# Kernel tuning notes

Measured on AMD Instinct MI355X. Metric: run time of the kernel, lower is better.

The kernel has to match this reference:

```python
import jax, jax.numpy as jnp
import numpy as np

WS = (7, 7, 7)
N = WS[0] * WS[1] * WS[2]          # 343 tokens per window
B, D, L, H = 128, 512, 6, 8
DH = D // H                        # 64
DFF = 4 * D
EPS = 1e-5


def _relative_position_index_3d(ws):
    d = np.arange(ws[0]); h = np.arange(ws[1]); w = np.arange(ws[2])
    coords = np.stack(np.meshgrid(d, h, w, indexing='ij'))      # [3, D, H, W]
    cf = coords.reshape(3, -1)                                   # [3, n]
    rel = cf[:, :, None] - cf[:, None, :]                        # [3, n, n]
    rel = rel.transpose(1, 2, 0).copy()                          # [n, n, 3]
    rel[:, :, 0] += ws[0] - 1
    rel[:, :, 1] += ws[1] - 1
    rel[:, :, 2] += ws[2] - 1
    rel[:, :, 0] *= (2 * ws[1] - 1) * (2 * ws[2] - 1)
    rel[:, :, 1] *= 2 * ws[2] - 1
    return rel.sum(-1).astype(np.int32)                          # [n, n]


def setup_inputs() -> dict:
    key = jax.random.key(0)
    ks = jax.random.split(key, 16)
    s = lambda d: 1.0 / np.sqrt(d)
    inp = {
        'x':    jax.random.normal(ks[0], (B, N, D), jnp.float32),
        'Wq':   jax.random.normal(ks[1], (L, D, D), jnp.float32) * s(D),
        'Wk':   jax.random.normal(ks[2], (L, D, D), jnp.float32) * s(D),
        'Wv':   jax.random.normal(ks[3], (L, D, D), jnp.float32) * s(D),
        'Wo':   jax.random.normal(ks[4], (L, D, D), jnp.float32) * s(D),
        'W1ff': jax.random.normal(ks[5], (L, D, DFF), jnp.float32) * s(D),
        'b1ff': jnp.zeros((L, DFF), jnp.float32),
        'W2ff': jax.random.normal(ks[6], (L, DFF, D), jnp.float32) * s(DFF),
        'b2ff': jnp.zeros((L, D), jnp.float32),
        'ln1_g': jnp.ones((L, D), jnp.float32),
        'ln1_b': jnp.zeros((L, D), jnp.float32),
        'ln2_g': jnp.ones((L, D), jnp.float32),
        'ln2_b': jnp.zeros((L, D), jnp.float32),
        'lnf_g': jnp.ones((D,), jnp.float32),
        'lnf_b': jnp.zeros((D,), jnp.float32),
        'rel_table': jax.random.normal(ks[7], ((2 * WS[0] - 1) * (2 * WS[1] - 1) * (2 * WS[2] - 1), H), jnp.float32) * 0.02,
        'cpb_w1': jax.random.normal(ks[8], (H, 512), jnp.float32) * s(H),
        'cpb_b1': jax.random.normal(ks[9], (512,), jnp.float32) * 0.02,
        'cpb_w2': jax.random.normal(ks[10], (512, H), jnp.float32) * s(512),
        'rel_index': jnp.asarray(_relative_position_index_3d(WS)),
    }
    return inp


def _layer_norm(x, g, b):
    mu = jnp.mean(x, -1, keepdims=True)
    xc = x - mu
    var = jnp.mean(xc * xc, -1, keepdims=True)
    return xc * jax.lax.rsqrt(var + EPS) * g + b


def _rel_pos_bias(rel_table, cpb_w1, cpb_b1, cpb_w2, rel_index):
    # cpb_mlp: Linear(H->512) + ReLU + Linear(512->H, no bias)
    t = jax.nn.relu(rel_table @ cpb_w1 + cpb_b1) @ cpb_w2        # [T, H]
    bias = t[rel_index.reshape(-1)].reshape(N, N, H)             # gather -> [n, n, H]
    return jnp.transpose(bias, (2, 0, 1))                        # [H, n, n]


def reference(x, Wq, Wk, Wv, Wo, W1ff, b1ff, W2ff, b2ff,
              ln1_g, ln1_b, ln2_g, ln2_b, lnf_g, lnf_b,
              rel_table, cpb_w1, cpb_b1, cpb_w2, rel_index):
    bias = _rel_pos_bias(rel_table, cpb_w1, cpb_b1, cpb_w2, rel_index)  # [H, n, n] shared across layers
    scale = DH ** -0.5
    for l in range(L):
        # --- attention block (pre-norm) ---
        h = _layer_norm(x, ln1_g[l], ln1_b[l])
        q = (h @ Wq[l]).reshape(B, N, H, DH)
        k = (h @ Wk[l]).reshape(B, N, H, DH)
        v = (h @ Wv[l]).reshape(B, N, H, DH)
        scores = jnp.einsum('bihd,bjhd->bhij', q, k) * scale + bias[None]
        attn = jax.nn.softmax(scores, axis=-1)
        o = jnp.einsum('bhij,bjhd->bihd', attn, v).reshape(B, N, D)
        x = x + o @ Wo[l]
        # --- feed-forward block (pre-norm) ---
        h = _layer_norm(x, ln2_g[l], ln2_b[l])
        x = x + jax.nn.gelu(h @ W1ff[l] + b1ff[l]) @ W2ff[l] + b2ff[l]
    return _layer_norm(x, lnf_g, lnf_b)
```

## Files before the change

### kernel.cpp

```cpp
#include <hip/hip_runtime.h>

typedef __attribute__((ext_vector_type(8))) short short8;
typedef __attribute__((ext_vector_type(4))) float fx4;
typedef __attribute__((ext_vector_type(4))) int ix4;

#define MFMA16(a, b, c) __builtin_amdgcn_mfma_f32_16x16x32_bf16((a), (b), (c), 0, 0, 0)

__device__ __forceinline__ short f2bf(float f) {
  unsigned u = __float_as_uint(f);
  u += 0x7fffu + ((u >> 16) & 1u);
  return (short)(u >> 16);
}
__device__ __forceinline__ float bf2f(short v) {
  return __uint_as_float(((unsigned)(unsigned short)v) << 16);
}
__device__ __forceinline__ void glds16(const short* g, short* l) {
  __builtin_amdgcn_global_load_lds((const __attribute__((address_space(1))) void*)g,
                                   (__attribute__((address_space(3))) void*)l, 16, 0, 0);
}
__device__ __forceinline__ unsigned lds_off(const void* p) {
  return (unsigned)(uintptr_t)(const __attribute__((address_space(3))) void*)p;
}
__device__ __forceinline__ ix4 ds_read128(unsigned addr) {
  ix4 r;
  asm volatile("ds_read_b128 %0, %1" : "=v"(r) : "v"(addr));
  return r;
}

__global__ __launch_bounds__(256)
void transpose_cvt(const float* __restrict__ W, short* __restrict__ Wt, int K, int N) {
  __shared__ float tile[64][65];
  const int kb = blockIdx.x * 64, nb = blockIdx.y * 64;
  const int t = threadIdx.x;
  const int tr = t >> 6, tc = t & 63;
#pragma unroll 4
  for (int i = 0; i < 16; i++) {
    int r = i * 4 + tr;
    tile[r][tc] = W[(size_t)(kb + r) * N + nb + tc];
  }
  __syncthreads();
#pragma unroll 4
  for (int i = 0; i < 16; i++) {
    int r = i * 4 + tr;
    Wt[(size_t)(nb + r) * K + kb + tc] = f2bf(tile[tc][r]);
  }
}

__global__ __launch_bounds__(256)
void cpb_kernel(const float* __restrict__ rt, const float* __restrict__ w1,
                const float* __restrict__ b1, const float* __restrict__ w2,
                float* __restrict__ tt) {
  const int id = blockIdx.x * 256 + threadIdx.x;
  if (id >= 2197 * 8) return;
  const int row = id >> 3, hh = id & 7;
  float r[8];
#pragma unroll
  for (int i = 0; i < 8; i++) r[i] = rt[row * 8 + i];
  float acc = 0.0f;
  for (int c = 0; c < 512; c++) {
    float s = b1[c];
#pragma unroll
    for (int i = 0; i < 8; i++) s += r[i] * w1[i * 512 + c];
    s = fmaxf(s, 0.0f);
    acc += s * w2[c * 8 + hh];
  }
  tt[id] = acc;
}

__global__ __launch_bounds__(256)
void build_biasfrag(const float* __restrict__ tt, const int* __restrict__ ridx,
                    short* __restrict__ biasb) {
  const int id = blockIdx.x * 256 + threadIdx.x;
  if (id >= 8 * 22 * 11 * 512) return;
  const int e = id & 7;
  const int lane = (id >> 3) & 63;
  const int rest = id >> 9;
  const int jp = rest % 11;
  const int rest2 = rest / 11;
  const int qt = rest2 % 22;
  const int h = rest2 / 22;
  const int q = qt * 16 + ((lane >> 4) << 2) + (e & 3);
  const int tok = (jp * 2 + (e >> 2)) * 16 + (lane & 15);
  float val = -1e30f;
  if (q < 343 && tok < 343) val = tt[ridx[q * 343 + tok] * 8 + h];
  biasb[id] = f2bf(val);
}

template <bool BF16OUT>
__global__ __launch_bounds__(256)
void ln_kernel(const float* x, const float* __restrict__ g,
               const float* __restrict__ bb, void* out) {
  const int row = blockIdx.x * 4 + (threadIdx.x >> 6);
  const int lane = threadIdx.x & 63;
  const float* xr = x + (size_t)row * 512 + lane * 8;
  fx4 va = *(const fx4*)xr;
  fx4 vb = *(const fx4*)(xr + 4);
  float s = va[0] + va[1] + va[2] + va[3] + vb[0] + vb[1] + vb[2] + vb[3];
#pragma unroll
  for (int d = 1; d < 64; d <<= 1) s += __shfl_xor(s, d);
  const float mu = s * (1.0f / 512.0f);
  float v[8];
#pragma unroll
  for (int i = 0; i < 4; i++) { v[i] = va[i] - mu; v[4 + i] = vb[i] - mu; }
  float s2 = 0.0f;
#pragma unroll
  for (int i = 0; i < 8; i++) s2 += v[i] * v[i];
#pragma unroll
  for (int d = 1; d < 64; d <<= 1) s2 += __shfl_xor(s2, d);
  const float rs = rsqrtf(s2 * (1.0f / 512.0f) + 1e-5f);
  fx4 ga = *(const fx4*)(g + lane * 8);
  fx4 gb = *(const fx4*)(g + lane * 8 + 4);
  fx4 ba = *(const fx4*)(bb + lane * 8);
  fx4 b2 = *(const fx4*)(bb + lane * 8 + 4);
  float o[8];
#pragma unroll
  for (int i = 0; i < 4; i++) {
    o[i] = v[i] * rs * ga[i] + ba[i];
    o[4 + i] = v[4 + i] * rs * gb[i] + b2[i];
  }
  if (BF16OUT) {
    short8 ov;
#pragma unroll
    for (int i = 0; i < 8; i++) ov[i] = f2bf(o[i]);
    *(short8*)((short*)out + (size_t)row * 512 + lane * 8) = ov;
  } else {
    float* op = (float*)out + (size_t)row * 512 + lane * 8;
    fx4 o1, o2;
#pragma unroll
    for (int i = 0; i < 4; i++) { o1[i] = o[i]; o2[i] = o[4 + i]; }
    *(fx4*)op = o1;
    *(fx4*)(op + 4) = o2;
  }
}

template <int EPI>
__global__ __launch_bounds__(256, 3)
void gemm_s(const short* __restrict__ A, const short* __restrict__ Bt,
            int N, int K, int nbn, int scaleN,
            const float* __restrict__ bias, const float* xres, void* out) {
  __shared__ short Al[3][4096];
  __shared__ short Bl[3][4096];
  const int nwg = gridDim.x;
  const int orig = blockIdx.x;
  const int qq = nwg >> 3, rr = nwg & 7, xc = orig & 7, o8 = orig >> 3;
  const int wgid = (xc < rr ? xc * (qq + 1) : rr * (qq + 1) + (xc - rr) * qq) + o8;
  const int m0 = (wgid / nbn) * 128, n0 = (wgid % nbn) * 128;
  const int t = threadIdx.x, lane = t & 63, wv = t >> 6;
  const int wm = (wv >> 1) * 64, wn = (wv & 1) * 64;
  const int lr = lane & 15, lg = lane >> 4;
  const int scol = ((lane & 3) * 8) ^ ((lane & 32) ? 16 : 0);
  const int srow = lane >> 2;
  const short* ag0 = A + (size_t)(m0 + wv * 32 + srow) * K + scol;
  const short* ag1 = A + (size_t)(m0 + wv * 32 + 16 + srow) * K + scol;
  const short* bg0 = Bt + (size_t)(n0 + wv * 32 + srow) * K + scol;
  const short* bg1 = Bt + (size_t)(n0 + wv * 32 + 16 + srow) * K + scol;
  const int cswz = (lg * 8) ^ ((lr & 8) ? 16 : 0);
  const unsigned abase = lds_off(&Al[0][0]);
  const unsigned bbase = lds_off(&Bl[0][0]);
  unsigned aoffB[4], boffB[4];
#pragma unroll
  for (int i = 0; i < 4; i++) {
    aoffB[i] = (((wv >> 1) * 4 + i) * 512 + lr * 32 + cswz) * 2u;
    boffB[i] = (((wv & 1) * 4 + i) * 512 + lr * 32 + cswz) * 2u;
  }
  fx4 acc[4][4] = {};
#define STAGE(KT, BUF)                              \
  do {                                              \
    const int off_ = (KT) * 32;                     \
    short* la_ = &Al[BUF][wv * 1024];               \
    short* lb_ = &Bl[BUF][wv * 1024];               \
    glds16(ag0 + off_, la_);                        \
    glds16(ag1 + off_, la_ + 512);                  \
    glds16(bg0 + off_, lb_);                        \
    glds16(bg1 + off_, lb_ + 512);                  \
  } while (0)
  const int nkt = K >> 5;
  STAGE(0, 0);
  STAGE(1, 1);
  int rb = 0;
  for (int kt = 0; kt < nkt; kt++) {
    if (kt + 1 < nkt)
      asm volatile("s_waitcnt vmcnt(4)" ::: "memory");
    else
      asm volatile("s_waitcnt vmcnt(0)" ::: "memory");
    __builtin_amdgcn_s_barrier();
    if (kt + 2 < nkt) {
      int sb = rb + 2;
      if (sb >= 3) sb -= 3;
      STAGE(kt + 2, sb);
    }
    const unsigned ab = abase + (unsigned)rb * 8192u;
    const unsigned bb_ = bbase + (unsigned)rb * 8192u;
    ix4 ar[4], br[4];
#pragma unroll
    for (int i = 0; i < 4; i++) ar[i] = ds_read128(ab + aoffB[i]);
#pragma unroll
    for (int i = 0; i < 4; i++) br[i] = ds_read128(bb_ + boffB[i]);
    asm volatile("s_waitcnt lgkmcnt(0)" ::: "memory");
    __builtin_amdgcn_sched_barrier(0);
#pragma unroll
    for (int mi = 0; mi < 4; mi++) {
      const short8 af = __builtin_bit_cast(short8, ar[mi]);
#pragma unroll
      for (int ni = 0; ni < 4; ni++)
        acc[mi][ni] = MFMA16(af, __builtin_bit_cast(short8, br[ni]), acc[mi][ni]);
    }
    rb = (rb + 1 < 3) ? rb + 1 : 0;
  }
#undef STAGE
#pragma unroll
  for (int mi = 0; mi < 4; mi++) {
#pragma unroll
    for (int ni = 0; ni < 4; ni++) {
#pragma unroll
      for (int r = 0; r < 4; r++) {
        const int row = m0 + wm + mi * 16 + lg * 4 + r;
        const int col = n0 + wn + ni * 16 + lr;
        const float vacc = acc[mi][ni][r];
        const size_t idx = (size_t)row * N + col;
        if (EPI == 0) {
          const float sc = (col < scaleN) ? 0.125f : 1.0f;
          ((short*)out)[idx] = f2bf(vacc * sc);
        } else if (EPI == 1) {
          ((float*)out)[idx] = xres[idx] + vacc;
        } else if (EPI == 2) {
          const float v = vacc + bias[col];
          const float tt = v * v;
          const float u2 = v * fmaf(tt, -0.0713548165f, -1.5957691216f);
          const float g = v * __builtin_amdgcn_rcpf(1.0f + __expf(u2));
          ((short*)out)[idx] = f2bf(g);
        } else {
          ((float*)out)[idx] = xres[idx] + vacc + bias[col];
        }
      }
    }
  }
}

__global__ __launch_bounds__(512, 1)
void attn_kernel(const short* __restrict__ qkv, const short* __restrict__ biasb,
                 short* __restrict__ obuf) {
  __shared__ short Kl[352][72];
  __shared__ short Vt[64][360];
  __shared__ short Pl[8][16][96];
  const int b = blockIdx.x >> 3, h = blockIdx.x & 7;
  const int t = threadIdx.x, lane = t & 63, wv = t >> 6;
  const int lr = lane & 15, lg = lane >> 4;
  const size_t base = (size_t)b * 343 * 1536 + h * 64;
  const short* qg = qkv + base;
  const short* kg = qkv + base + 512;
  const short* vg = qkv + base + 1024;
  for (int c = t; c < 352 * 8; c += 512) {
    const int tok = c >> 3, d8 = (c & 7) * 8;
    const int ts = tok < 343 ? tok : 342;
    short8 kvv = *(const short8*)(kg + (size_t)ts * 1536 + d8);
    short8 vvv = *(const short8*)(vg + (size_t)ts * 1536 + d8);
    *(short8*)&Kl[tok][d8] = kvv;
#pragma unroll
    for (int j = 0; j < 8; j++) Vt[d8 + j][tok] = vvv[j];
  }
  __syncthreads();
  for (int qt = wv; qt < 22; qt += 8) {
    const int q0 = qt * 16;
    const int qr = q0 + lr;
    const int qs = qr < 343 ? qr : 342;
    short8 qf0 = *(const short8*)(qg + (size_t)qs * 1536 + lg * 8);
    short8 qf1 = *(const short8*)(qg + (size_t)qs * 1536 + 32 + lg * 8);
    fx4 s[22];
#pragma unroll
    for (int j = 0; j < 22; j++) {
      short8 kf0 = *(const short8*)&Kl[j * 16 + lr][lg * 8];
      short8 kf1 = *(const short8*)&Kl[j * 16 + lr][32 + lg * 8];
      fx4 z = {0.0f, 0.0f, 0.0f, 0.0f};
      z = MFMA16(qf0, kf0, z);
      z = MFMA16(qf1, kf1, z);
      s[j] = z;
    }
    const short* bp = biasb + (size_t)((h * 22 + qt) * 11) * 512 + lane * 8;
#pragma unroll
    for (int jp = 0; jp < 11; jp++) {
      short8 bb = *(const short8*)(bp + jp * 512);
#pragma unroll
      for (int r = 0; r < 4; r++) {
        s[2 * jp][r] += bf2f(bb[r]);
        s[2 * jp + 1][r] += bf2f(bb[4 + r]);
      }
    }
    float mx[4] = {-1e30f, -1e30f, -1e30f, -1e30f};
#pragma unroll
    for (int j = 0; j < 22; j++)
#pragma unroll
      for (int r = 0; r < 4; r++) mx[r] = fmaxf(mx[r], s[j][r]);
#pragma unroll
    for (int r = 0; r < 4; r++) {
      float m = mx[r];
      m = fmaxf(m, __shfl_xor(m, 1));
      m = fmaxf(m, __shfl_xor(m, 2));
      m = fmaxf(m, __shfl_xor(m, 4));
      m = fmaxf(m, __shfl_xor(m, 8));
      mx[r] = m;
    }
    float sm[4] = {0.0f, 0.0f, 0.0f, 0.0f};
#pragma unroll
    for (int j = 0; j < 22; j++)
#pragma unroll
      for (int r = 0; r < 4; r++) {
        const float p = __expf(s[j][r] - mx[r]);
        s[j][r] = p;
        sm[r] += p;
      }
#pragma unroll
    for (int r = 0; r < 4; r++) {
      float ss = sm[r];
      ss += __shfl_xor(ss, 1);
      ss += __shfl_xor(ss, 2);
      ss += __shfl_xor(ss, 4);
      ss += __shfl_xor(ss, 8);
      sm[r] = 1.0f / ss;
    }
    fx4 oacc[4] = {};
#pragma unroll
    for (int c = 0; c < 4; c++) {
      const int nj = (c < 3) ? 6 : 4;
#pragma unroll
      for (int j = 0; j < 6; j++) {
        if (j < nj) {
#pragma unroll
          for (int r = 0; r < 4; r++)
            Pl[wv][lg * 4 + r][j * 16 + lr] = f2bf(s[c * 6 + j][r] * sm[r]);
        }
      }
      const int nk = (c < 3) ? 3 : 2;
#pragma unroll
      for (int ks = 0; ks < 3; ks++) {
        if (ks < nk) {
          short8 pb = *(const short8*)&Pl[wv][lr][ks * 32 + lg * 8];
#pragma unroll
          for (int mi = 0; mi < 4; mi++) {
            short8 vva = *(const short8*)&Vt[mi * 16 + lr][c * 96 + ks * 32 + lg * 8];
            oacc[mi] = MFMA16(vva, pb, oacc[mi]);
          }
        }
      }
    }
    if (qr < 343) {
#pragma unroll
      for (int mi = 0; mi < 4; mi++)
#pragma unroll
        for (int r = 0; r < 4; r++) {
          const int dh = mi * 16 + lg * 4 + r;
          obuf[(size_t)(b * 343 + qr) * 512 + h * 64 + dh] = f2bf(oacc[mi][r]);
        }
    }
  }
}

extern "C" void kernel_launch(void* const* d_in, const int* in_sizes, int n_in,
                              void* d_out, int out_size, void* d_ws, size_t ws_size,
                              hipStream_t stream) {
  const float* x_in = (const float*)d_in[0];
  const float* Wq = (const float*)d_in[1];
  const float* Wk = (const float*)d_in[2];
  const float* Wv = (const float*)d_in[3];
  const float* Wo = (const float*)d_in[4];
  const float* W1 = (const float*)d_in[5];
  const float* b1 = (const float*)d_in[6];
  const float* W2 = (const float*)d_in[7];
  const float* b2 = (const float*)d_in[8];
  const float* ln1g = (const float*)d_in[9];
  const float* ln1b = (const float*)d_in[10];
  const float* ln2g = (const float*)d_in[11];
  const float* ln2b = (const float*)d_in[12];
  const float* lnfg = (const float*)d_in[13];
  const float* lnfb = (const float*)d_in[14];
  const float* rtab = (const float*)d_in[15];
  const float* cw1 = (const float*)d_in[16];
  const float* cb1 = (const float*)d_in[17];
  const float* cw2 = (const float*)d_in[18];
  const int* ridx = (const int*)d_in[19];
  float* xout = (float*)d_out;

  char* p = (char*)d_ws;
  short* wt = (short*)p;      p += 37748736;
  short* hbuf = (short*)p;    p += 44957696;
  char* big = p;              p += 179830784;
  short* biasb = (short*)p;   p += 1982464;
  float* tt = (float*)p;      p += 70304;
  short* qkvbuf = (short*)big;
  short* obuf = (short*)(big + 134873088);
  short* mid = (short*)big;

  cpb_kernel<<<(2197 * 8 + 255) / 256, 256, 0, stream>>>(rtab, cw1, cb1, cw2, tt);
  build_biasfrag<<<(8 * 22 * 11 * 512 + 255) / 256, 256, 0, stream>>>(tt, ridx, biasb);

  for (int l = 0; l < 6; l++) {
    const size_t wl = (size_t)l * 3145728;
    transpose_cvt<<<dim3(8, 8), 256, 0, stream>>>(Wq + (size_t)l * 262144, wt + wl, 512, 512);
    transpose_cvt<<<dim3(8, 8), 256, 0, stream>>>(Wk + (size_t)l * 262144, wt + wl + 262144, 512, 512);
    transpose_cvt<<<dim3(8, 8), 256, 0, stream>>>(Wv + (size_t)l * 262144, wt + wl + 524288, 512, 512);
    transpose_cvt<<<dim3(8, 8), 256, 0, stream>>>(Wo + (size_t)l * 262144, wt + wl + 786432, 512, 512);
    transpose_cvt<<<dim3(8, 32), 256, 0, stream>>>(W1 + (size_t)l * 1048576, wt + wl + 1048576, 512, 2048);
    transpose_cvt<<<dim3(32, 8), 256, 0, stream>>>(W2 + (size_t)l * 1048576, wt + wl + 2097152, 2048, 512);
  }

  for (int l = 0; l < 6; l++) {
    const size_t wl = (size_t)l * 3145728;
    const float* xsrc = (l == 0) ? x_in : xout;
    ln_kernel<true><<<10976, 256, 0, stream>>>(xsrc, ln1g + l * 512, ln1b + l * 512, hbuf);
    gemm_s<0><<<343 * 12, 256, 0, stream>>>(hbuf, wt + wl, 1536, 512, 12, 512, nullptr, nullptr, qkvbuf);
    attn_kernel<<<1024, 512, 0, stream>>>(qkvbuf, biasb, obuf);
    gemm_s<1><<<343 * 4, 256, 0, stream>>>(obuf, wt + wl + 786432, 512, 512, 4, 0, nullptr, xsrc, xout);
    ln_kernel<true><<<10976, 256, 0, stream>>>(xout, ln2g + l * 512, ln2b + l * 512, hbuf);
    gemm_s<2><<<343 * 16, 256, 0, stream>>>(hbuf, wt + wl + 1048576, 2048, 512, 16, 0, b1 + l * 2048, nullptr, mid);
    gemm_s<3><<<343 * 4, 256, 0, stream>>>(mid, wt + wl + 2097152, 512, 2048, 4, 0, b2 + l * 512, xout, xout);
  }
  ln_kernel<false><<<10976, 256, 0, stream>>>(xout, lnfg, lnfb, xout);
}
```

Baseline: 4.069 ms.

## Make GEMM staging wave-private with 4-deep pipeline and barrier-free loop

```diff
diff --git a/kernel.cpp b/kernel.cpp
--- a/kernel.cpp
+++ b/kernel.cpp
@@ -26,6 +26,9 @@
   asm volatile("ds_read_b128 %0, %1" : "=v"(r) : "v"(addr));
   return r;
 }
+#define LGKM(N)                                             \
+  asm volatile("s_waitcnt lgkmcnt(" #N ")" ::: "memory");   \
+  __builtin_amdgcn_sched_barrier(0)
 
 __global__ __launch_bounds__(256)
 void transpose_cvt(const float* __restrict__ W, short* __restrict__ Wt, int K, int N) {
@@ -134,12 +137,11 @@
 }
 
 template <int EPI>
-__global__ __launch_bounds__(256, 3)
-void gemm_s(const short* __restrict__ A, const short* __restrict__ Bt,
+__global__ __launch_bounds__(256)
+void gemm_w(const short* __restrict__ A, const short* __restrict__ Bt,
             int N, int K, int nbn, int scaleN,
             const float* __restrict__ bias, const float* xres, void* out) {
-  __shared__ short Al[3][4096];
-  __shared__ short Bl[3][4096];
+  __shared__ short lds_all[4][16384];
   const int nwg = gridDim.x;
   const int orig = blockIdx.x;
   const int qq = nwg >> 3, rr = nwg & 7, xc = orig & 7, o8 = orig >> 3;
@@ -150,62 +152,93 @@
   const int lr = lane & 15, lg = lane >> 4;
   const int scol = ((lane & 3) * 8) ^ ((lane & 32) ? 16 : 0);
   const int srow = lane >> 2;
-  const short* ag0 = A + (size_t)(m0 + wv * 32 + srow) * K + scol;
-  const short* ag1 = A + (size_t)(m0 + wv * 32 + 16 + srow) * K + scol;
-  const short* bg0 = Bt + (size_t)(n0 + wv * 32 + srow) * K + scol;
-  const short* bg1 = Bt + (size_t)(n0 + wv * 32 + 16 + srow) * K + scol;
+  const short* agp[4];
+  const short* bgp[4];
+#pragma unroll
+  for (int c = 0; c < 4; c++) {
+    agp[c] = A + (size_t)(m0 + wm + c * 16 + srow) * K + scol;
+    bgp[c] = Bt + (size_t)(n0 + wn + c * 16 + srow) * K + scol;
+  }
   const int cswz = (lg * 8) ^ ((lr & 8) ? 16 : 0);
-  const unsigned abase = lds_off(&Al[0][0]);
-  const unsigned bbase = lds_off(&Bl[0][0]);
-  unsigned aoffB[4], boffB[4];
+  const unsigned wbase = lds_off(&lds_all[wv][0]);
+  unsigned aoff[4], boff[4];
 #pragma unroll
   for (int i = 0; i < 4; i++) {
-    aoffB[i] = (((wv >> 1) * 4 + i) * 512 + lr * 32 + cswz) * 2u;
-    boffB[i] = (((wv & 1) * 4 + i) * 512 + lr * 32 + cswz) * 2u;
+    aoff[i] = (unsigned)(i * 512 + (lr * 32 + cswz)) * 2u;
+    boff[i] = (unsigned)(2048 + i * 512 + (lr * 32 + cswz)) * 2u;
   }
   fx4 acc[4][4] = {};
-#define STAGE(KT, BUF)                              \
-  do {                                              \
-    const int off_ = (KT) * 32;                     \
-    short* la_ = &Al[BUF][wv * 1024];               \
-    short* lb_ = &Bl[BUF][wv * 1024];               \
-    glds16(ag0 + off_, la_);                        \
-    glds16(ag1 + off_, la_ + 512);                  \
-    glds16(bg0 + off_, lb_);                        \
-    glds16(bg1 + off_, lb_ + 512);                  \
+#define STAGE(KT)                                      \
+  do {                                                 \
+    const size_t koff = (size_t)(KT) * 32;             \
+    short* ld = &lds_all[wv][((KT) & 3) * 4096];       \
+    glds16(agp[0] + koff, ld);                         \
+    glds16(agp[1] + koff, ld + 512);                   \
+    glds16(agp[2] + koff, ld + 1024);                  \
+    glds16(agp[3] + koff, ld + 1536);                  \
+    glds16(bgp[0] + koff, ld + 2048);                  \
+    glds16(bgp[1] + koff, ld + 2560);                  \
+    glds16(bgp[2] + koff, ld + 3072);                  \
+    glds16(bgp[3] + koff, ld + 3584);                  \
   } while (0)
   const int nkt = K >> 5;
-  STAGE(0, 0);
-  STAGE(1, 1);
-  int rb = 0;
+  STAGE(0);
+  STAGE(1);
+  STAGE(2);
   for (int kt = 0; kt < nkt; kt++) {
-    if (kt + 1 < nkt)
-      asm volatile("s_waitcnt vmcnt(4)" ::: "memory");
+    if (kt + 2 < nkt)
+      asm volatile("s_waitcnt vmcnt(16)" ::: "memory");
+    else if (kt + 1 < nkt)
+      asm volatile("s_waitcnt vmcnt(8)" ::: "memory");
     else
       asm volatile("s_waitcnt vmcnt(0)" ::: "memory");
-    __builtin_amdgcn_s_barrier();
-    if (kt + 2 < nkt) {
-      int sb = rb + 2;
-      if (sb >= 3) sb -= 3;
-      STAGE(kt + 2, sb);
-    }
-    const unsigned ab = abase + (unsigned)rb * 8192u;
-    const unsigned bb_ = bbase + (unsigned)rb * 8192u;
-    ix4 ar[4], br[4];
-#pragma unroll
-    for (int i = 0; i < 4; i++) ar[i] = ds_read128(ab + aoffB[i]);
-#pragma unroll
-    for (int i = 0; i < 4; i++) br[i] = ds_read128(bb_ + boffB[i]);
-    asm volatile("s_waitcnt lgkmcnt(0)" ::: "memory");
-    __builtin_amdgcn_sched_barrier(0);
-#pragma unroll
-    for (int mi = 0; mi < 4; mi++) {
-      const short8 af = __builtin_bit_cast(short8, ar[mi]);
-#pragma unroll
-      for (int ni = 0; ni < 4; ni++)
-        acc[mi][ni] = MFMA16(af, __builtin_bit_cast(short8, br[ni]), acc[mi][ni]);
-    }
-    rb = (rb + 1 < 3) ? rb + 1 : 0;
+    if (kt + 3 < nkt) STAGE(kt + 3);
+    const unsigned bufb = wbase + (unsigned)(kt & 3) * 8192u;
+    ix4 a0 = ds_read128(bufb + aoff[0]);
+    ix4 b0 = ds_read128(bufb + boff[0]);
+    ix4 b1 = ds_read128(bufb + boff[1]);
+    ix4 b2 = ds_read128(bufb + boff[2]);
+    ix4 b3 = ds_read128(bufb + boff[3]);
+    ix4 a1 = ds_read128(bufb + aoff[1]);
+    ix4 a2 = ds_read128(bufb + aoff[2]);
+    ix4 a3 = ds_read128(bufb + aoff[3]);
+    const short8 A0 = __builtin_bit_cast(short8, a0);
+    const short8 B0 = __builtin_bit_cast(short8, b0);
+    const short8 B1 = __builtin_bit_cast(short8, b1);
+    const short8 B2 = __builtin_bit_cast(short8, b2);
+    const short8 B3 = __builtin_bit_cast(short8, b3);
+    LGKM(6);
+    acc[0][0] = MFMA16(A0, B0, acc[0][0]);
+    LGKM(5);
+    acc[0][1] = MFMA16(A0, B1, acc[0][1]);
+    LGKM(4);
+    acc[0][2] = MFMA16(A0, B2, acc[0][2]);
+    LGKM(3);
+    acc[0][3] = MFMA16(A0, B3, acc[0][3]);
+    LGKM(2);
+    {
+      const short8 A1 = __builtin_bit_cast(short8, a1);
+      acc[1][0] = MFMA16(A1, B0, acc[1][0]);
+      acc[1][1] = MFMA16(A1, B1, acc[1][1]);
+      acc[1][2] = MFMA16(A1, B2, acc[1][2]);
+      acc[1][3] = MFMA16(A1, B3, acc[1][3]);
+    }
+    LGKM(1);
+    {
+      const short8 A2 = __builtin_bit_cast(short8, a2);
+      acc[2][0] = MFMA16(A2, B0, acc[2][0]);
+      acc[2][1] = MFMA16(A2, B1, acc[2][1]);
+      acc[2][2] = MFMA16(A2, B2, acc[2][2]);
+      acc[2][3] = MFMA16(A2, B3, acc[2][3]);
+    }
+    LGKM(0);
+    {
+      const short8 A3 = __builtin_bit_cast(short8, a3);
+      acc[3][0] = MFMA16(A3, B0, acc[3][0]);
+      acc[3][1] = MFMA16(A3, B1, acc[3][1]);
+      acc[3][2] = MFMA16(A3, B2, acc[3][2]);
+      acc[3][3] = MFMA16(A3, B3, acc[3][3]);
+    }
   }
 #undef STAGE
 #pragma unroll
@@ -407,12 +440,12 @@
     const size_t wl = (size_t)l * 3145728;
     const float* xsrc = (l == 0) ? x_in : xout;
     ln_kernel<true><<<10976, 256, 0, stream>>>(xsrc, ln1g + l * 512, ln1b + l * 512, hbuf);
-    gemm_s<0><<<343 * 12, 256, 0, stream>>>(hbuf, wt + wl, 1536, 512, 12, 512, nullptr, nullptr, qkvbuf);
+    gemm_w<0><<<343 * 12, 256, 0, stream>>>(hbuf, wt + wl, 1536, 512, 12, 512, nullptr, nullptr, qkvbuf);
     attn_kernel<<<1024, 512, 0, stream>>>(qkvbuf, biasb, obuf);
-    gemm_s<1><<<343 * 4, 256, 0, stream>>>(obuf, wt + wl + 786432, 512, 512, 4, 0, nullptr, xsrc, xout);
+    gemm_w<1><<<343 * 4, 256, 0, stream>>>(obuf, wt + wl + 786432, 512, 512, 4, 0, nullptr, xsrc, xout);
     ln_kernel<true><<<10976, 256, 0, stream>>>(xout, ln2g + l * 512, ln2b + l * 512, hbuf);
-    gemm_s<2><<<343 * 16, 256, 0, stream>>>(hbuf, wt + wl + 1048576, 2048, 512, 16, 0, b1 + l * 2048, nullptr, mid);
-    gemm_s<3><<<343 * 4, 256, 0, stream>>>(mid, wt + wl + 2097152, 512, 2048, 4, 0, b2 + l * 512, xout, xout);
+    gemm_w<2><<<343 * 16, 256, 0, stream>>>(hbuf, wt + wl + 1048576, 2048, 512, 16, 0, b1 + l * 2048, nullptr, mid);
+    gemm_w<3><<<343 * 4, 256, 0, stream>>>(mid, wt + wl + 2097152, 512, 2048, 4, 0, b2 + l * 512, xout, xout);
   }
   ln_kernel<false><<<10976, 256, 0, stream>>>(xout, lnfg, lnfb, xout);
 }
```

Result: slower. 6.005 ms (+47.6%).

## Enlarge GEMM tile to 256x128 with staggered LDS-read waits

Applied to the files above, without the earlier changes.

```diff
diff --git a/kernel.cpp b/kernel.cpp
--- a/kernel.cpp
+++ b/kernel.cpp
@@ -26,6 +26,9 @@
   asm volatile("ds_read_b128 %0, %1" : "=v"(r) : "v"(addr));
   return r;
 }
+#define LGKM(N)                                             \
+  asm volatile("s_waitcnt lgkmcnt(" #N ")" ::: "memory");   \
+  __builtin_amdgcn_sched_barrier(0)
 
 __global__ __launch_bounds__(256)
 void transpose_cvt(const float* __restrict__ W, short* __restrict__ Wt, int K, int N) {
@@ -134,45 +137,49 @@
 }
 
 template <int EPI>
-__global__ __launch_bounds__(256, 3)
-void gemm_s(const short* __restrict__ A, const short* __restrict__ Bt,
-            int N, int K, int nbn, int scaleN,
+__global__ __launch_bounds__(256, 2)
+void gemm_b(const short* __restrict__ A, const short* __restrict__ Bt,
+            int M, int N, int K, int nbn, int scaleN,
             const float* __restrict__ bias, const float* xres, void* out) {
-  __shared__ short Al[3][4096];
-  __shared__ short Bl[3][4096];
+  __shared__ short lds3[3][12288];
   const int nwg = gridDim.x;
   const int orig = blockIdx.x;
   const int qq = nwg >> 3, rr = nwg & 7, xc = orig & 7, o8 = orig >> 3;
   const int wgid = (xc < rr ? xc * (qq + 1) : rr * (qq + 1) + (xc - rr) * qq) + o8;
-  const int m0 = (wgid / nbn) * 128, n0 = (wgid % nbn) * 128;
+  const int m0 = (wgid / nbn) * 256, n0 = (wgid % nbn) * 128;
   const int t = threadIdx.x, lane = t & 63, wv = t >> 6;
-  const int wm = (wv >> 1) * 64, wn = (wv & 1) * 64;
+  const int wave_m = wv >> 1, wave_n = wv & 1;
   const int lr = lane & 15, lg = lane >> 4;
   const int scol = ((lane & 3) * 8) ^ ((lane & 32) ? 16 : 0);
   const int srow = lane >> 2;
-  const short* ag0 = A + (size_t)(m0 + wv * 32 + srow) * K + scol;
-  const short* ag1 = A + (size_t)(m0 + wv * 32 + 16 + srow) * K + scol;
-  const short* bg0 = Bt + (size_t)(n0 + wv * 32 + srow) * K + scol;
-  const short* bg1 = Bt + (size_t)(n0 + wv * 32 + 16 + srow) * K + scol;
+  const short* gsrc[6];
+#pragma unroll
+  for (int j = 0; j < 6; j++) {
+    const int c = wv * 6 + j;
+    if (c < 16) {
+      int rw = m0 + c * 16 + srow;
+      if (rw > M - 1) rw = M - 1;
+      gsrc[j] = A + (size_t)rw * K + scol;
+    } else {
+      gsrc[j] = Bt + (size_t)(n0 + (c - 16) * 16 + srow) * K + scol;
+    }
+  }
   const int cswz = (lg * 8) ^ ((lr & 8) ? 16 : 0);
-  const unsigned abase = lds_off(&Al[0][0]);
-  const unsigned bbase = lds_off(&Bl[0][0]);
-  unsigned aoffB[4], boffB[4];
-#pragma unroll
-  for (int i = 0; i < 4; i++) {
-    aoffB[i] = (((wv >> 1) * 4 + i) * 512 + lr * 32 + cswz) * 2u;
-    boffB[i] = (((wv & 1) * 4 + i) * 512 + lr * 32 + cswz) * 2u;
-  }
-  fx4 acc[4][4] = {};
-#define STAGE(KT, BUF)                              \
-  do {                                              \
-    const int off_ = (KT) * 32;                     \
-    short* la_ = &Al[BUF][wv * 1024];               \
-    short* lb_ = &Bl[BUF][wv * 1024];               \
-    glds16(ag0 + off_, la_);                        \
-    glds16(ag1 + off_, la_ + 512);                  \
-    glds16(bg0 + off_, lb_);                        \
-    glds16(bg1 + off_, lb_ + 512);                  \
+  const unsigned base0 = lds_off(&lds3[0][0]);
+  unsigned aoff[8], boff[4];
+#pragma unroll
+  for (int i = 0; i < 8; i++)
+    aoff[i] = (unsigned)((wave_m * 8 + i) * 512 + lr * 32 + cswz) * 2u;
+#pragma unroll
+  for (int i = 0; i < 4; i++)
+    boff[i] = (unsigned)(8192 + (wave_n * 4 + i) * 512 + lr * 32 + cswz) * 2u;
+  fx4 acc[8][4] = {};
+#define STAGE(KT, BUF)                                    \
+  do {                                                    \
+    const size_t koff = (size_t)(KT) * 32;                \
+    short* ld = &lds3[BUF][wv * 3072];                    \
+    _Pragma("unroll") for (int j_ = 0; j_ < 6; j_++)      \
+        glds16(gsrc[j_] + koff, ld + j_ * 512);           \
   } while (0)
   const int nkt = K >> 5;
   STAGE(0, 0);
@@ -180,7 +187,7 @@
   int rb = 0;
   for (int kt = 0; kt < nkt; kt++) {
     if (kt + 1 < nkt)
-      asm volatile("s_waitcnt vmcnt(4)" ::: "memory");
+      asm volatile("s_waitcnt vmcnt(6)" ::: "memory");
     else
       asm volatile("s_waitcnt vmcnt(0)" ::: "memory");
     __builtin_amdgcn_s_barrier();
@@ -189,33 +196,60 @@
       if (sb >= 3) sb -= 3;
       STAGE(kt + 2, sb);
     }
-    const unsigned ab = abase + (unsigned)rb * 8192u;
-    const unsigned bb_ = bbase + (unsigned)rb * 8192u;
-    ix4 ar[4], br[4];
-#pragma unroll
-    for (int i = 0; i < 4; i++) ar[i] = ds_read128(ab + aoffB[i]);
-#pragma unroll
-    for (int i = 0; i < 4; i++) br[i] = ds_read128(bb_ + boffB[i]);
-    asm volatile("s_waitcnt lgkmcnt(0)" ::: "memory");
-    __builtin_amdgcn_sched_barrier(0);
-#pragma unroll
-    for (int mi = 0; mi < 4; mi++) {
-      const short8 af = __builtin_bit_cast(short8, ar[mi]);
-#pragma unroll
-      for (int ni = 0; ni < 4; ni++)
-        acc[mi][ni] = MFMA16(af, __builtin_bit_cast(short8, br[ni]), acc[mi][ni]);
-    }
+    const unsigned bb_ = base0 + (unsigned)rb * 24576u;
+    ix4 a0 = ds_read128(bb_ + aoff[0]);
+    ix4 b0 = ds_read128(bb_ + boff[0]);
+    ix4 b1 = ds_read128(bb_ + boff[1]);
+    ix4 b2 = ds_read128(bb_ + boff[2]);
+    ix4 b3 = ds_read128(bb_ + boff[3]);
+    ix4 a1 = ds_read128(bb_ + aoff[1]);
+    ix4 a2 = ds_read128(bb_ + aoff[2]);
+    ix4 a3 = ds_read128(bb_ + aoff[3]);
+    ix4 a4 = ds_read128(bb_ + aoff[4]);
+    ix4 a5 = ds_read128(bb_ + aoff[5]);
+    ix4 a6 = ds_read128(bb_ + aoff[6]);
+    ix4 a7 = ds_read128(bb_ + aoff[7]);
+    const short8 B0 = __builtin_bit_cast(short8, b0);
+    const short8 B1 = __builtin_bit_cast(short8, b1);
+    const short8 B2 = __builtin_bit_cast(short8, b2);
+    const short8 B3 = __builtin_bit_cast(short8, b3);
+#define ROW(mi, av)                                                  \
+  {                                                                  \
+    const short8 Af = __builtin_bit_cast(short8, av);                \
+    acc[mi][0] = MFMA16(Af, B0, acc[mi][0]);                         \
+    acc[mi][1] = MFMA16(Af, B1, acc[mi][1]);                         \
+    acc[mi][2] = MFMA16(Af, B2, acc[mi][2]);                         \
+    acc[mi][3] = MFMA16(Af, B3, acc[mi][3]);                         \
+  }
+    LGKM(7);
+    ROW(0, a0);
+    LGKM(6);
+    ROW(1, a1);
+    LGKM(5);
+    ROW(2, a2);
+    LGKM(4);
+    ROW(3, a3);
+    LGKM(3);
+    ROW(4, a4);
+    LGKM(2);
+    ROW(5, a5);
+    LGKM(1);
+    ROW(6, a6);
+    LGKM(0);
+    ROW(7, a7);
+#undef ROW
     rb = (rb + 1 < 3) ? rb + 1 : 0;
   }
 #undef STAGE
 #pragma unroll
-  for (int mi = 0; mi < 4; mi++) {
+  for (int mi = 0; mi < 8; mi++) {
 #pragma unroll
     for (int ni = 0; ni < 4; ni++) {
 #pragma unroll
       for (int r = 0; r < 4; r++) {
-        const int row = m0 + wm + mi * 16 + lg * 4 + r;
-        const int col = n0 + wn + ni * 16 + lr;
+        const int row = m0 + wave_m * 128 + mi * 16 + lg * 4 + r;
+        if (row >= M) continue;
+        const int col = n0 + wave_n * 64 + ni * 16 + lr;
         const float vacc = acc[mi][ni][r];
         const size_t idx = (size_t)row * N + col;
         if (EPI == 0) {
@@ -390,6 +424,8 @@
   short* obuf = (short*)(big + 134873088);
   short* mid = (short*)big;
 
+  const int M = 43904;
+
   cpb_kernel<<<(2197 * 8 + 255) / 256, 256, 0, stream>>>(rtab, cw1, cb1, cw2, tt);
   build_biasfrag<<<(8 * 22 * 11 * 512 + 255) / 256, 256, 0, stream>>>(tt, ridx, biasb);
 
@@ -407,12 +443,12 @@
     const size_t wl = (size_t)l * 3145728;
     const float* xsrc = (l == 0) ? x_in : xout;
     ln_kernel<true><<<10976, 256, 0, stream>>>(xsrc, ln1g + l * 512, ln1b + l * 512, hbuf);
-    gemm_s<0><<<343 * 12, 256, 0, stream>>>(hbuf, wt + wl, 1536, 512, 12, 512, nullptr, nullptr, qkvbuf);
+    gemm_b<0><<<172 * 12, 256, 0, stream>>>(hbuf, wt + wl, M, 1536, 512, 12, 512, nullptr, nullptr, qkvbuf);
     attn_kernel<<<1024, 512, 0, stream>>>(qkvbuf, biasb, obuf);
-    gemm_s<1><<<343 * 4, 256, 0, stream>>>(obuf, wt + wl + 786432, 512, 512, 4, 0, nullptr, xsrc, xout);
+    gemm_b<1><<<172 * 4, 256, 0, stream>>>(obuf, wt + wl + 786432, M, 512, 512, 4, 0, nullptr, xsrc, xout);
     ln_kernel<true><<<10976, 256, 0, stream>>>(xout, ln2g + l * 512, ln2b + l * 512, hbuf);
-    gemm_s<2><<<343 * 16, 256, 0, stream>>>(hbuf, wt + wl + 1048576, 2048, 512, 16, 0, b1 + l * 2048, nullptr, mid);
-    gemm_s<3><<<343 * 4, 256, 0, stream>>>(mid, wt + wl + 2097152, 512, 2048, 4, 0, b2 + l * 512, xout, xout);
+    gemm_b<2><<<172 * 16, 256, 0, stream>>>(hbuf, wt + wl + 1048576, M, 2048, 512, 16, 0, b1 + l * 2048, nullptr, mid);
+    gemm_b<3><<<172 * 4, 256, 0, stream>>>(mid, wt + wl + 2097152, M, 512, 2048, 4, 0, b2 + l * 512, xout, xout);
   }
   ln_kernel<false><<<10976, 256, 0, stream>>>(xout, lnfg, lnfb, xout);
 }
```

After: 5.132 ms. 26.1% more time.
